# Optimization experiments

Hardware: AMD Instinct MI355X
Metric: run time of the kernel (lower is better)

The kernel has to match this reference:

```python
import jax, jax.numpy as jnp
import numpy as np

H = 2048        # hidden_size
E = 8           # num_experts
TOPK = 2
I = 1408        # moe_intermediate_size
IS = 5632       # shared_expert_intermediate_size
NORM_TOPK = True


def setup_inputs() -> dict:
    key = jax.random.key(0)
    ks = jax.random.split(key, 9)
    s = lambda k, shape: jax.random.normal(k, shape, dtype=jnp.float32) * (1.0 / np.sqrt(shape[-2] if len(shape) > 1 else shape[-1]))
    return {
        "hidden_states": jax.random.normal(ks[0], (1, 512, H), dtype=jnp.float32),
        "gate_w": jax.random.normal(ks[1], (E, H), dtype=jnp.float32) * 0.02,   # router Linear(H->E), no bias
        "w_gate": s(ks[2], (E, H, I)),   # expert gate_proj
        "w_up": s(ks[3], (E, H, I)),     # expert up_proj
        "w_down": s(ks[4], (E, I, H)),   # expert down_proj
        "sh_gate_w": s(ks[5], (H, IS)),  # shared expert gate_proj
        "sh_up_w": s(ks[6], (H, IS)),    # shared expert up_proj
        "sh_down_w": s(ks[7], (IS, H)),  # shared expert down_proj
        "shexp_gate_w": jax.random.normal(ks[8], (H, 1), dtype=jnp.float32) * 0.02,  # shared_expert_gate Linear(H->1)
    }


def reference(hidden_states, gate_w, w_gate, w_up, w_down,
              sh_gate_w, sh_up_w, sh_down_w, shexp_gate_w):
    B, S, _ = hidden_states.shape
    x = hidden_states.reshape(-1, H)                      # [T, H]
    T = x.shape[0]

    # --- router: softmax over all experts, then top-k (moe_gating_topk_softmax) ---
    router_logits = x @ gate_w.T                          # [T, E]
    probs = jax.nn.softmax(router_logits, axis=-1)
    routing_weights, selected_experts = jax.lax.top_k(probs, TOPK)  # [T, K]
    if NORM_TOPK:
        routing_weights = routing_weights / jnp.sum(routing_weights, axis=-1, keepdims=True)

    # dense combine weights: combine[t, e] = routing weight if expert e selected for token t else 0
    combine = jnp.zeros((T, E), dtype=x.dtype)
    combine = combine.at[jnp.arange(T)[:, None], selected_experts].set(routing_weights)

    # --- experts: SwiGLU MLP per expert, vectorized over E ---
    g = jnp.einsum('th,ehi->tei', x, w_gate)              # [T, E, I]
    u = jnp.einsum('th,ehi->tei', x, w_up)                # [T, E, I]
    h = jax.nn.silu(g) * u                                # [T, E, I]
    expert_out = jnp.einsum('tei,eih,te->th', h, w_down, combine)  # weighted scatter-add

    # --- shared expert with sigmoid gate ---
    sh = jax.nn.silu(x @ sh_gate_w) * (x @ sh_up_w)       # [T, IS]
    shared_out = (sh @ sh_down_w) * jax.nn.sigmoid(x @ shexp_gate_w)  # [T, H]

    out = (expert_out + shared_out).reshape(B, S, H)
    return (out, router_logits)
```

## Files before the change

### kernel.cpp

```cpp
#include <hip/hip_runtime.h>
#include <hip/hip_bf16.h>

#define NT  512
#define NH  2048
#define NE  8
#define NI  1408
#define NIS 5632

typedef __bf16 bf16x8 __attribute__((ext_vector_type(8)));
typedef float  f32x4  __attribute__((ext_vector_type(4)));

#define GLDS(gp, lp) __builtin_amdgcn_global_load_lds( \
    (const __attribute__((address_space(1))) void*)(gp), \
    (__attribute__((address_space(3))) void*)(lp), 16, 0, 0)

static constexpr size_t WS_XBF  = 0;
static constexpr size_t WS_SEL  = WS_XBF + (size_t)NT*NH*2;
static constexpr size_t WS_WTS  = WS_SEL + 4096;
static constexpr size_t WS_CNT  = WS_WTS + 4096;
static constexpr size_t WS_OFFE = WS_CNT + 32;
static constexpr size_t WS_TOK  = WS_OFFE + 32;
static constexpr size_t WS_PWT  = WS_TOK + 4096;
static constexpr size_t WS_SLOT = WS_PWT + 4096;
static constexpr size_t WS_G    = WS_SLOT + 4096;
static constexpr size_t WS_U    = WS_G   + (size_t)1024*NI*2;
static constexpr size_t WS_HBF  = WS_U   + (size_t)1024*NI*2;
static constexpr size_t WS_PAIR = WS_HBF + (size_t)1024*NI*2;
static constexpr size_t WS_SHG  = WS_PAIR+ (size_t)1024*NH*2;
static constexpr size_t WS_SHU  = WS_SHG + (size_t)NT*NIS*2;
static constexpr size_t WS_SHBF = WS_SHU + (size_t)NT*NIS*2;
static constexpr size_t WS_SHP  = WS_SHBF+ (size_t)NT*NIS*2;

__global__ void router_kernel(const float* __restrict__ x, const float* __restrict__ gw,
                              float* __restrict__ out_logits,
                              int* __restrict__ sel, float* __restrict__ wts)
{
    int w    = threadIdx.x >> 6;
    int lane = threadIdx.x & 63;
    int t    = blockIdx.x * 4 + w;
    int e    = lane & 7, c = lane >> 3;
    const float* xr = x  + (size_t)t * NH + c * 256;
    const float* gr = gw + (size_t)e * NH + c * 256;
    float acc = 0.f;
    #pragma unroll 8
    for (int it = 0; it < 64; ++it) {
        float4 xv = *(const float4*)(xr + it*4);
        float4 gv = *(const float4*)(gr + it*4);
        acc += xv.x*gv.x + xv.y*gv.y + xv.z*gv.z + xv.w*gv.w;
    }
    acc += __shfl_xor(acc, 8);
    acc += __shfl_xor(acc, 16);
    acc += __shfl_xor(acc, 32);
    if (lane < 8) out_logits[(size_t)t * NE + e] = acc;

    float l[8];
    #pragma unroll
    for (int j = 0; j < 8; ++j) l[j] = __shfl(acc, j);
    if (lane == 0) {
        int i1 = 0;
        #pragma unroll
        for (int j = 1; j < 8; ++j) if (l[j] > l[i1]) i1 = j;
        int i2 = -1;
        #pragma unroll
        for (int j = 0; j < 8; ++j) {
            if (j == i1) continue;
            if (i2 < 0 || l[j] > l[i2]) i2 = j;
        }
        float d  = expf(l[i2] - l[i1]);
        float w1 = 1.f / (1.f + d);
        float w2 = 1.f - w1;
        sel[2*t]   = i1;  sel[2*t+1] = i2;
        wts[2*t]   = w1;  wts[2*t+1] = w2;
    }
}

__global__ void bucket_kernel(const int* __restrict__ sel, const float* __restrict__ wts,
                              int* __restrict__ cnt, int* __restrict__ offe,
                              int* __restrict__ tok, float* __restrict__ pwt,
                              int* __restrict__ slot)
{
    int tid  = threadIdx.x;
    int wid  = tid >> 6;
    int lane = tid & 63;
    __shared__ int scnt[8], soff[8];

    unsigned long long masks[16];
    int total = 0;
    #pragma unroll
    for (int c = 0; c < 16; ++c) {
        int idx = c * 64 + lane;
        int s = sel[idx];
        unsigned long long m = __ballot(s == wid);
        masks[c] = m;
        total += __popcll(m);
    }
    if (lane == 0) { scnt[wid] = total; cnt[wid] = total; }
    __syncthreads();
    if (tid == 0) {
        int s = 0;
        #pragma unroll
        for (int j = 0; j < 8; ++j) { soff[j] = s; offe[j] = s; s += scnt[j]; }
    }
    __syncthreads();
    int pfx = soff[wid];
    unsigned long long below = (lane == 63) ? ~0ull >> 1 : ((1ull << lane) - 1);
    #pragma unroll
    for (int c = 0; c < 16; ++c) {
        int idx = c * 64 + lane;
        unsigned long long m = masks[c];
        if ((m >> lane) & 1ull) {
            int rank = pfx + (int)__popcll(m & below);
            tok[rank]  = idx >> 1;
            pwt[rank]  = wts[idx];
            slot[idx]  = rank;
        }
        pfx += (int)__popcll(m);
    }
}

__global__ void cast_kernel(const float* __restrict__ src, __bf16* __restrict__ dst, long long n)
{
    long long i = ((long long)blockIdx.x * blockDim.x + threadIdx.x) * 4;
    if (i >= n) return;
    float4 v = *(const float4*)(src + i);
    __bf16 o[4] = { (__bf16)v.x, (__bf16)v.y, (__bf16)v.z, (__bf16)v.w };
    *(uint2*)(dst + i) = *(const uint2*)o;
}

__global__ void silu_fused_kernel(const __bf16* __restrict__ g1, const __bf16* __restrict__ u1,
                                  __bf16* __restrict__ h1, long long n1,
                                  const __bf16* __restrict__ g2, const __bf16* __restrict__ u2,
                                  __bf16* __restrict__ h2, long long n2)
{
    long long i = ((long long)blockIdx.x * blockDim.x + threadIdx.x) * 8;
    const __bf16 *g, *u; __bf16* h; long long idx;
    if (i < n1)           { g = g1; u = u1; h = h1; idx = i; }
    else if (i < n1 + n2) { g = g2; u = u2; h = h2; idx = i - n1; }
    else return;
    uint4 gv = *(const uint4*)(g + idx);
    uint4 uv = *(const uint4*)(u + idx);
    const __bf16* gp = (const __bf16*)&gv;
    const __bf16* up = (const __bf16*)&uv;
    __bf16 o[8];
    #pragma unroll
    for (int j = 0; j < 8; ++j) {
        float x = (float)gp[j];
        float y = x / (1.f + __expf(-x)) * (float)up[j];
        o[j] = (__bf16)y;
    }
    *(uint4*)(h + idx) = *(const uint4*)o;
}

template<int NK, int LDB, bool GATHER>
__device__ __forceinline__ void gemm_core(char* __restrict__ smem,
    const __bf16* __restrict__ A, int lda,
    const float* __restrict__ B,
    __bf16* __restrict__ C, int ldc,
    int rows, int base, const int* __restrict__ tok, int m0, int n0)
{
    const int tid  = threadIdx.x;
    const int lane = tid & 63;
    const int wid  = tid >> 6;
    const int wr   = wid >> 1, wc = wid & 1;

    const int rs0 = (wid*2 + 0)*16 + (lane >> 2);
    const int rs1 = (wid*2 + 1)*16 + (lane >> 2);
    const int cch = lane & 3;
    int ga0 = m0 + rs0, ga1 = m0 + rs1;
    int ar0, ar1;
    if (GATHER) {
        ar0 = tok[base + (ga0 < rows ? ga0 : 0)];
        ar1 = tok[base + (ga1 < rows ? ga1 : 0)];
    } else {
        ar0 = base + (ga0 < rows ? ga0 : 0);
        ar1 = base + (ga1 < rows ? ga1 : 0);
    }
    const __bf16* a0p = A + (size_t)ar0 * lda + (cch ^ (rs0 & 3)) * 8;
    const __bf16* a1p = A + (size_t)ar1 * lda + (cch ^ (rs1 & 3)) * 8;

#define AGLDS(slot, t)                                               \
    {                                                                \
        char* d0 = smem + (slot)*8192 + (wid*2 + 0)*1024;            \
        char* d1 = smem + (slot)*8192 + (wid*2 + 1)*1024;            \
        GLDS(a0p + (size_t)(t)*32, d0);                              \
        GLDS(a1p + (size_t)(t)*32, d1);                              \
    }

    const int cn  = tid & 127;
    const int ckh = tid >> 7;
    const int csw = (cn >> 1) & 3;
    const float* bp = B + (size_t)(ckh * 16) * LDB + n0 + cn;
    char* bbuf0 = smem + 24576;
    char* bbuf1 = smem + 32768;

#define BLOAD(R, t)                                                  \
    {                                                                \
        const float* bq = bp + (size_t)(t) * 32 * LDB;               \
        _Pragma("unroll")                                            \
        for (int j = 0; j < 16; ++j) R[j] = bq[(size_t)j * LDB];     \
    }

#define CONVERT(R, bbase)                                            \
    {                                                                \
        __bf16 ob[16];                                               \
        _Pragma("unroll")                                            \
        for (int j = 0; j < 16; ++j) ob[j] = (__bf16)R[j];           \
        *(uint4*)((bbase) + cn*64 + (((ckh*2 + 0) ^ csw) * 16)) = ((const uint4*)ob)[0]; \
        *(uint4*)((bbase) + cn*64 + (((ckh*2 + 1) ^ csw) * 16)) = ((const uint4*)ob)[1]; \
    }

    const int fr = lane & 15, fq = lane >> 4;
    const int aoff = (wr*64 + fr)*64 + ((fq ^ (fr & 3)) * 16);
    const int boff = (wc*64 + fr)*64 + ((fq ^ ((fr >> 1) & 3)) * 16);

    f32x4 acc[4][4];
    #pragma unroll
    for (int i = 0; i < 4; ++i)
        #pragma unroll
        for (int j = 0; j < 4; ++j) acc[i][j] = f32x4{0.f,0.f,0.f,0.f};

#define MFMAS(slot, bbase)                                           \
    {                                                                \
        const char* Ab = smem + (slot)*8192;                         \
        bf16x8 af[4], bfr[4];                                        \
        _Pragma("unroll")                                            \
        for (int m = 0; m < 4; ++m) af[m]  = *(const bf16x8*)(Ab + aoff + m*1024); \
        _Pragma("unroll")                                            \
        for (int n = 0; n < 4; ++n) bfr[n] = *(const bf16x8*)((bbase) + boff + n*1024); \
        __builtin_amdgcn_s_setprio(1);                               \
        _Pragma("unroll")                                            \
        for (int m = 0; m < 4; ++m)                                  \
            _Pragma("unroll")                                        \
            for (int n = 0; n < 4; ++n)                              \
                acc[m][n] = __builtin_amdgcn_mfma_f32_16x16x32_bf16(af[m], bfr[n], acc[m][n], 0, 0, 0); \
        __builtin_amdgcn_s_setprio(0);                               \
    }

    float b0[16], b1[16];

    BLOAD(b0, 0); AGLDS(0, 0);
    BLOAD(b1, 1); AGLDS(1, 1);
    asm volatile("s_waitcnt vmcnt(18)" ::: "memory");
    CONVERT(b0, bbuf0);
    asm volatile("s_waitcnt lgkmcnt(0)" ::: "memory");
    __builtin_amdgcn_s_barrier();

    int sA = 0, sB = 1, sC = 2;
    #pragma unroll 1
    for (int t = 0; t < NK; t += 2) {
        if (t + 2 < NK) { BLOAD(b0, t + 2); AGLDS(sC, t + 2); }
        __builtin_amdgcn_sched_barrier(0);
        MFMAS(sA, bbuf0);
        __builtin_amdgcn_sched_barrier(0);
        if (t + 2 < NK) asm volatile("s_waitcnt vmcnt(18)" ::: "memory");
        else            asm volatile("s_waitcnt vmcnt(0)"  ::: "memory");
        CONVERT(b1, bbuf1);
        asm volatile("s_waitcnt lgkmcnt(0)" ::: "memory");
        __builtin_amdgcn_s_barrier();

        if (t + 3 < NK) { BLOAD(b1, t + 3); AGLDS(sA, t + 3); }
        __builtin_amdgcn_sched_barrier(0);
        MFMAS(sB, bbuf1);
        __builtin_amdgcn_sched_barrier(0);
        if (t + 2 < NK) {
            if (t + 3 < NK) asm volatile("s_waitcnt vmcnt(18)" ::: "memory");
            else            asm volatile("s_waitcnt vmcnt(0)"  ::: "memory");
            CONVERT(b0, bbuf0);
        }
        asm volatile("s_waitcnt lgkmcnt(0)" ::: "memory");
        __builtin_amdgcn_s_barrier();

        int tmp = sA; sA = sC; sC = sB; sB = tmp;
    }
#undef AGLDS
#undef BLOAD
#undef CONVERT
#undef MFMAS

    __bf16* ep = (__bf16*)(smem + wid * 9216);
    #pragma unroll
    for (int m = 0; m < 4; ++m)
        #pragma unroll
        for (int n = 0; n < 4; ++n)
            #pragma unroll
            for (int q = 0; q < 4; ++q)
                ep[(m*16 + fq*4 + q)*72 + n*16 + fr] = (__bf16)acc[m][n][q];

    const int grow = m0 + wr*64 + lane;
    if (grow < rows) {
        __bf16* cp = C + (size_t)(base + grow) * ldc + n0 + wc*64;
        const __bf16* rp = ep + lane * 72;
        #pragma unroll
        for (int j = 0; j < 8; ++j)
            *(uint4*)(cp + j*8) = *(const uint4*)(rp + j*8);
    }
}

__launch_bounds__(256, 3)
__global__ void gemm_p1(const __bf16* __restrict__ xbf,
                        const float* __restrict__ w_gate, const float* __restrict__ w_up,
                        const float* __restrict__ sh_gate, const float* __restrict__ sh_up,
                        __bf16* __restrict__ gbuf, __bf16* __restrict__ ubuf,
                        __bf16* __restrict__ shg, __bf16* __restrict__ shu,
                        const int* __restrict__ cnt, const int* __restrict__ offe,
                        const int* __restrict__ tok)
{
    __shared__ alignas(16) char smem[40960];
    int g = blockIdx.x;
    int x = g & 7;
    int j = g >> 3;
    if (j < 88) {
        int gu = j / 44;
        int r  = j % 44;
        int n  = r % 11;
        int m  = r / 11;
        int rows = cnt[x], base = offe[x];
        int m0 = m * 128; if (m0 >= rows) return;
        const float* B = (gu == 0 ? w_gate : w_up) + (size_t)x * NH * NI;
        __bf16* C = (gu == 0 ? gbuf : ubuf);
        gemm_core<NH/32, NI, true>(smem, xbf, NH, B, C, NI,
                                   rows, base, tok, m0, n * 128);
    } else {
        int s = j - 88;
        int z = s / 24;
        int rem = s % 24;
        int i = rem >> 2;
        int m = rem & 3;
        int n = x + 8 * i;
        if (n >= 44) return;
        const float* B = (z == 0 ? sh_gate : sh_up);
        __bf16* C = (z == 0 ? shg : shu);
        gemm_core<NH/32, NIS, false>(smem, xbf, NH, B, C, NIS,
                                     NT, 0, nullptr, m * 128, n * 128);
    }
}

__launch_bounds__(256, 3)
__global__ void gemm_p3(const __bf16* __restrict__ hbf, const __bf16* __restrict__ shbf,
                        const float* __restrict__ w_down, const float* __restrict__ sh_down,
                        __bf16* __restrict__ pair, __bf16* __restrict__ shp,
                        const int* __restrict__ cnt, const int* __restrict__ offe)
{
    __shared__ alignas(16) char smem[40960];
    int g = blockIdx.x;
    int x = g & 7;
    int j = g >> 3;
    if (j < 64) {
        int n = j % 16;
        int m = j / 16;
        int rows = cnt[x], base = offe[x];
        int m0 = m * 128; if (m0 >= rows) return;
        gemm_core<NI/32, NH, false>(smem, hbf, NI, w_down + (size_t)x * NI * NH,
                                    pair, NH, rows, base, nullptr, m0, n * 128);
    } else {
        int s = j - 64;
        int q = s >> 3;
        int rem = s & 7;
        int i = rem >> 2;
        int m = rem & 3;
        int n = x + 8 * i;
        gemm_core<NI/32, NH, false>(smem, shbf + q * NI, NIS,
                                    sh_down + (size_t)q * NI * NH,
                                    shp + (size_t)q * NT * NH, NH,
                                    NT, 0, nullptr, m * 128, n * 128);
    }
}

__global__ void combine_kernel(const float* __restrict__ x, const float* __restrict__ shexp_w,
                               const __bf16* __restrict__ shp, const __bf16* __restrict__ pair_out,
                               const int* __restrict__ slot, const float* __restrict__ wts,
                               float* __restrict__ out)
{
    int t = blockIdx.x;
    int tid = threadIdx.x;
    const float* xr = x + (size_t)t * NH;

    float p = 0.f;
    #pragma unroll
    for (int j = 0; j < 8; ++j) {
        int k = tid * 8 + j;
        p += xr[k] * shexp_w[k];
    }
    __shared__ float red[256];
    red[tid] = p;
    __syncthreads();
    for (int s = 128; s > 0; s >>= 1) {
        if (tid < s) red[tid] += red[tid + s];
        __syncthreads();
    }
    float sig = 1.f / (1.f + expf(-red[0]));

    int   s0 = slot[2*t],   s1 = slot[2*t+1];
    float w0 = wts[2*t],    w1 = wts[2*t+1];
    const __bf16* pr0 = pair_out + (size_t)s0 * NH;
    const __bf16* pr1 = pair_out + (size_t)s1 * NH;
    const __bf16* sd  = shp + (size_t)t * NH;
    float* orow = out + (size_t)t * NH;
    const size_t PS = (size_t)NT * NH;
    for (int n = tid; n < NH; n += 256) {
        float sdv = (float)sd[n] + (float)sd[n + PS] + (float)sd[n + 2*PS] + (float)sd[n + 3*PS];
        orow[n] = sdv * sig + w0 * (float)pr0[n] + w1 * (float)pr1[n];
    }
}

extern "C" void kernel_launch(void* const* d_in, const int* in_sizes, int n_in,
                              void* d_out, int out_size, void* d_ws, size_t ws_size,
                              hipStream_t stream)
{
    const float* x       = (const float*)d_in[0];
    const float* gate_w  = (const float*)d_in[1];
    const float* w_gate  = (const float*)d_in[2];
    const float* w_up    = (const float*)d_in[3];
    const float* w_down  = (const float*)d_in[4];
    const float* sh_gate = (const float*)d_in[5];
    const float* sh_up   = (const float*)d_in[6];
    const float* sh_down = (const float*)d_in[7];
    const float* shexp_g = (const float*)d_in[8];

    float* out        = (float*)d_out;
    float* out_logits = out + (size_t)NT * NH;

    char* ws = (char*)d_ws;
    __bf16* xbf  = (__bf16*)(ws + WS_XBF);
    int*    sel  = (int*)  (ws + WS_SEL);
    float*  wts  = (float*)(ws + WS_WTS);
    int*    cnt  = (int*)  (ws + WS_CNT);
    int*    offe = (int*)  (ws + WS_OFFE);
    int*    tok  = (int*)  (ws + WS_TOK);
    float*  pwt  = (float*)(ws + WS_PWT);
    int*    slot = (int*)  (ws + WS_SLOT);
    __bf16* gbuf = (__bf16*)(ws + WS_G);
    __bf16* ubuf = (__bf16*)(ws + WS_U);
    __bf16* hbf  = (__bf16*)(ws + WS_HBF);
    __bf16* pair = (__bf16*)(ws + WS_PAIR);
    __bf16* shg  = (__bf16*)(ws + WS_SHG);
    __bf16* shu  = (__bf16*)(ws + WS_SHU);
    __bf16* shbf = (__bf16*)(ws + WS_SHBF);
    __bf16* shp  = (__bf16*)(ws + WS_SHP);
    (void)pwt; (void)in_sizes; (void)n_in; (void)out_size; (void)ws_size;

    router_kernel<<<dim3(128), dim3(256), 0, stream>>>(x, gate_w, out_logits, sel, wts);
    bucket_kernel<<<dim3(1), dim3(512), 0, stream>>>(sel, wts, cnt, offe, tok, pwt, slot);
    cast_kernel<<<dim3(1024), dim3(256), 0, stream>>>(x, xbf, (long long)NT * NH);

    gemm_p1<<<dim3(1088), dim3(256), 0, stream>>>(
        xbf, w_gate, w_up, sh_gate, sh_up, gbuf, ubuf, shg, shu, cnt, offe, tok);

    silu_fused_kernel<<<dim3(2112), dim3(256), 0, stream>>>(
        gbuf, ubuf, hbf, (long long)1024 * NI,
        shg, shu, shbf, (long long)NT * NIS);

    gemm_p3<<<dim3(768), dim3(256), 0, stream>>>(
        hbf, shbf, w_down, sh_down, pair, shp, cnt, offe);

    combine_kernel<<<dim3(NT), dim3(256), 0, stream>>>(
        x, shexp_g, shp, pair, slot, wts, out);
}
```

Measured before the change: 199.6 us.

## Split-K the first GEMM phase in two and vectorize fp32 weight loads

The gate/up GEMMs (expert and shared) now split the K dimension into two halves, doubling the grid and writing bf16 partial sums to doubled workspace buffers. The SiLU kernel sums the two partials before applying the activation. Separately, the B-tile loader switches from 16 scalar strided loads per thread to 4 float4 loads with a new LDS store pattern, which lowers the outstanding-load counts in the waits. This aims for more parallelism and fewer memory instructions, at the cost of extra partial-result traffic and an extra bf16 rounding of the partial sums.

```diff
diff --git a/kernel.cpp b/kernel.cpp
--- a/kernel.cpp
+++ b/kernel.cpp
@@ -23,12 +23,12 @@
 static constexpr size_t WS_PWT  = WS_TOK + 4096;
 static constexpr size_t WS_SLOT = WS_PWT + 4096;
 static constexpr size_t WS_G    = WS_SLOT + 4096;
-static constexpr size_t WS_U    = WS_G   + (size_t)1024*NI*2;
-static constexpr size_t WS_HBF  = WS_U   + (size_t)1024*NI*2;
+static constexpr size_t WS_U    = WS_G   + (size_t)2*1024*NI*2;
+static constexpr size_t WS_HBF  = WS_U   + (size_t)2*1024*NI*2;
 static constexpr size_t WS_PAIR = WS_HBF + (size_t)1024*NI*2;
 static constexpr size_t WS_SHG  = WS_PAIR+ (size_t)1024*NH*2;
-static constexpr size_t WS_SHU  = WS_SHG + (size_t)NT*NIS*2;
-static constexpr size_t WS_SHBF = WS_SHU + (size_t)NT*NIS*2;
+static constexpr size_t WS_SHU  = WS_SHG + (size_t)2*NT*NIS*2;
+static constexpr size_t WS_SHBF = WS_SHU + (size_t)2*NT*NIS*2;
 static constexpr size_t WS_SHP  = WS_SHBF+ (size_t)NT*NIS*2;
 
 __global__ void router_kernel(const float* __restrict__ x, const float* __restrict__ gw,
@@ -128,24 +128,29 @@
 }
 
 __global__ void silu_fused_kernel(const __bf16* __restrict__ g1, const __bf16* __restrict__ u1,
-                                  __bf16* __restrict__ h1, long long n1,
+                                  __bf16* __restrict__ h1, long long n1, size_t ps1,
                                   const __bf16* __restrict__ g2, const __bf16* __restrict__ u2,
-                                  __bf16* __restrict__ h2, long long n2)
+                                  __bf16* __restrict__ h2, long long n2, size_t ps2)
 {
     long long i = ((long long)blockIdx.x * blockDim.x + threadIdx.x) * 8;
-    const __bf16 *g, *u; __bf16* h; long long idx;
-    if (i < n1)           { g = g1; u = u1; h = h1; idx = i; }
-    else if (i < n1 + n2) { g = g2; u = u2; h = h2; idx = i - n1; }
+    const __bf16 *g, *u; __bf16* h; long long idx; size_t ps;
+    if (i < n1)           { g = g1; u = u1; h = h1; idx = i;      ps = ps1; }
+    else if (i < n1 + n2) { g = g2; u = u2; h = h2; idx = i - n1; ps = ps2; }
     else return;
-    uint4 gv = *(const uint4*)(g + idx);
-    uint4 uv = *(const uint4*)(u + idx);
-    const __bf16* gp = (const __bf16*)&gv;
-    const __bf16* up = (const __bf16*)&uv;
+    uint4 gv0 = *(const uint4*)(g + idx);
+    uint4 gv1 = *(const uint4*)(g + idx + ps);
+    uint4 uv0 = *(const uint4*)(u + idx);
+    uint4 uv1 = *(const uint4*)(u + idx + ps);
+    const __bf16* gp0 = (const __bf16*)&gv0;
+    const __bf16* gp1 = (const __bf16*)&gv1;
+    const __bf16* up0 = (const __bf16*)&uv0;
+    const __bf16* up1 = (const __bf16*)&uv1;
     __bf16 o[8];
     #pragma unroll
     for (int j = 0; j < 8; ++j) {
-        float x = (float)gp[j];
-        float y = x / (1.f + __expf(-x)) * (float)up[j];
+        float xg = (float)gp0[j] + (float)gp1[j];
+        float xu = (float)up0[j] + (float)up1[j];
+        float y = xg / (1.f + __expf(-xg)) * xu;
         o[j] = (__bf16)y;
     }
     *(uint4*)(h + idx) = *(const uint4*)o;
@@ -186,10 +191,11 @@
         GLDS(a1p + (size_t)(t)*32, d1);                              \
     }
 
-    const int cn  = tid & 127;
-    const int ckh = tid >> 7;
-    const int csw = (cn >> 1) & 3;
-    const float* bp = B + (size_t)(ckh * 16) * LDB + n0 + cn;
+    const int cn4 = (tid & 31) * 4;
+    const int kr4 = (tid >> 5) * 4;
+    const int kck = kr4 >> 3;
+    const int kh  = (kr4 >> 2) & 1;
+    const float* bp = B + (size_t)kr4 * LDB + n0 + cn4;
     char* bbuf0 = smem + 24576;
     char* bbuf1 = smem + 32768;
 
@@ -197,16 +203,21 @@
     {                                                                \
         const float* bq = bp + (size_t)(t) * 32 * LDB;               \
         _Pragma("unroll")                                            \
-        for (int j = 0; j < 16; ++j) R[j] = bq[(size_t)j * LDB];     \
+        for (int j = 0; j < 4; ++j)                                  \
+            R[j] = *(const float4*)(bq + (size_t)j * LDB);           \
     }
 
 #define CONVERT(R, bbase)                                            \
     {                                                                \
-        __bf16 ob[16];                                               \
         _Pragma("unroll")                                            \
-        for (int j = 0; j < 16; ++j) ob[j] = (__bf16)R[j];           \
-        *(uint4*)((bbase) + cn*64 + (((ckh*2 + 0) ^ csw) * 16)) = ((const uint4*)ob)[0]; \
-        *(uint4*)((bbase) + cn*64 + (((ckh*2 + 1) ^ csw) * 16)) = ((const uint4*)ob)[1]; \
+        for (int c = 0; c < 4; ++c) {                                \
+            __bf16 ob[4];                                            \
+            _Pragma("unroll")                                        \
+            for (int j = 0; j < 4; ++j)                              \
+                ob[j] = (__bf16)(((const float*)(R))[j*4 + c]);      \
+            int col = cn4 + c;                                       \
+            *(uint2*)((bbase) + col*64 + ((kck ^ ((col>>1)&3)) * 16) + kh*8) = *(const uint2*)ob; \
+        }                                                            \
     }
 
     const int fr = lane & 15, fq = lane >> 4;
@@ -236,11 +247,11 @@
         __builtin_amdgcn_s_setprio(0);                               \
     }
 
-    float b0[16], b1[16];
+    float4 b0[4], b1[4];
 
     BLOAD(b0, 0); AGLDS(0, 0);
     BLOAD(b1, 1); AGLDS(1, 1);
-    asm volatile("s_waitcnt vmcnt(18)" ::: "memory");
+    asm volatile("s_waitcnt vmcnt(6)" ::: "memory");
     CONVERT(b0, bbuf0);
     asm volatile("s_waitcnt lgkmcnt(0)" ::: "memory");
     __builtin_amdgcn_s_barrier();
@@ -252,8 +263,8 @@
         __builtin_amdgcn_sched_barrier(0);
         MFMAS(sA, bbuf0);
         __builtin_amdgcn_sched_barrier(0);
-        if (t + 2 < NK) asm volatile("s_waitcnt vmcnt(18)" ::: "memory");
-        else            asm volatile("s_waitcnt vmcnt(0)"  ::: "memory");
+        if (t + 2 < NK) asm volatile("s_waitcnt vmcnt(6)" ::: "memory");
+        else            asm volatile("s_waitcnt vmcnt(0)" ::: "memory");
         CONVERT(b1, bbuf1);
         asm volatile("s_waitcnt lgkmcnt(0)" ::: "memory");
         __builtin_amdgcn_s_barrier();
@@ -263,8 +274,8 @@
         MFMAS(sB, bbuf1);
         __builtin_amdgcn_sched_barrier(0);
         if (t + 2 < NK) {
-            if (t + 3 < NK) asm volatile("s_waitcnt vmcnt(18)" ::: "memory");
-            else            asm volatile("s_waitcnt vmcnt(0)"  ::: "memory");
+            if (t + 3 < NK) asm volatile("s_waitcnt vmcnt(6)" ::: "memory");
+            else            asm volatile("s_waitcnt vmcnt(0)" ::: "memory");
             CONVERT(b0, bbuf0);
         }
         asm volatile("s_waitcnt lgkmcnt(0)" ::: "memory");
@@ -309,29 +320,33 @@
     int g = blockIdx.x;
     int x = g & 7;
     int j = g >> 3;
-    if (j < 88) {
-        int gu = j / 44;
-        int r  = j % 44;
-        int n  = r % 11;
-        int m  = r / 11;
+    if (j < 176) {
+        int gu = j / 88;
+        int r  = j % 88;
+        int k2 = r / 44;
+        int rr = r % 44;
+        int n  = rr % 11;
+        int m  = rr / 11;
         int rows = cnt[x], base = offe[x];
         int m0 = m * 128; if (m0 >= rows) return;
-        const float* B = (gu == 0 ? w_gate : w_up) + (size_t)x * NH * NI;
-        __bf16* C = (gu == 0 ? gbuf : ubuf);
-        gemm_core<NH/32, NI, true>(smem, xbf, NH, B, C, NI,
-                                   rows, base, tok, m0, n * 128);
+        const float* B = (gu == 0 ? w_gate : w_up) + (size_t)x * NH * NI + (size_t)k2 * 1024 * NI;
+        __bf16* C = (gu == 0 ? gbuf : ubuf) + (size_t)k2 * 1024 * NI;
+        gemm_core<32, NI, true>(smem, xbf + k2 * 1024, NH, B, C, NI,
+                                rows, base, tok, m0, n * 128);
     } else {
-        int s = j - 88;
-        int z = s / 24;
-        int rem = s % 24;
-        int i = rem >> 2;
-        int m = rem & 3;
+        int s = j - 176;
+        int z = s / 48;
+        int rem = s % 48;
+        int k2 = rem / 24;
+        int rem2 = rem % 24;
+        int i = rem2 >> 2;
+        int m = rem2 & 3;
         int n = x + 8 * i;
         if (n >= 44) return;
-        const float* B = (z == 0 ? sh_gate : sh_up);
-        __bf16* C = (z == 0 ? shg : shu);
-        gemm_core<NH/32, NIS, false>(smem, xbf, NH, B, C, NIS,
-                                     NT, 0, nullptr, m * 128, n * 128);
+        const float* B = (z == 0 ? sh_gate : sh_up) + (size_t)k2 * 1024 * NIS;
+        __bf16* C = (z == 0 ? shg : shu) + (size_t)k2 * NT * NIS;
+        gemm_core<32, NIS, false>(smem, xbf + k2 * 1024, NH, B, C, NIS,
+                                  NT, 0, nullptr, m * 128, n * 128);
     }
 }
 
@@ -443,12 +458,12 @@
     bucket_kernel<<<dim3(1), dim3(512), 0, stream>>>(sel, wts, cnt, offe, tok, pwt, slot);
     cast_kernel<<<dim3(1024), dim3(256), 0, stream>>>(x, xbf, (long long)NT * NH);
 
-    gemm_p1<<<dim3(1088), dim3(256), 0, stream>>>(
+    gemm_p1<<<dim3(2176), dim3(256), 0, stream>>>(
         xbf, w_gate, w_up, sh_gate, sh_up, gbuf, ubuf, shg, shu, cnt, offe, tok);
 
     silu_fused_kernel<<<dim3(2112), dim3(256), 0, stream>>>(
-        gbuf, ubuf, hbf, (long long)1024 * NI,
-        shg, shu, shbf, (long long)NT * NIS);
+        gbuf, ubuf, hbf, (long long)1024 * NI, (size_t)1024 * NI,
+        shg, shu, shbf, (long long)NT * NIS, (size_t)NT * NIS);
 
     gemm_p3<<<dim3(768), dim3(256), 0, stream>>>(
         hbf, shbf, w_down, sh_down, pair, shp, cnt, offe);
```

Result: slower. 214.7 us (+7.6%).

## Use 256-row tiles for shared-expert GEMMs and halve down-proj split-K

Applied to the files above, without the earlier changes.

Adds a gemm_core256 variant that computes 256x128 output tiles, so each fp32 weight tile loaded and converted to bf16 is reused across twice as many token rows. This is meant to halve the weight traffic and conversion work of the shared-expert GEMMs. The shared down projection now splits K into 2 parts instead of 4, so the combine kernel sums two partials. LDS grows to 64KB and launch bounds drop to 2 blocks per CU, which lowers occupancy and adds register pressure for all GEMM blocks in both kernels, including the routed-expert ones.

```diff
diff --git a/kernel.cpp b/kernel.cpp
--- a/kernel.cpp
+++ b/kernel.cpp
@@ -253,7 +253,7 @@
         MFMAS(sA, bbuf0);
         __builtin_amdgcn_sched_barrier(0);
         if (t + 2 < NK) asm volatile("s_waitcnt vmcnt(18)" ::: "memory");
-        else            asm volatile("s_waitcnt vmcnt(0)"  ::: "memory");
+        else            asm volatile("s_waitcnt vmcnt(0)" ::: "memory");
         CONVERT(b1, bbuf1);
         asm volatile("s_waitcnt lgkmcnt(0)" ::: "memory");
         __builtin_amdgcn_s_barrier();
@@ -264,7 +264,7 @@
         __builtin_amdgcn_sched_barrier(0);
         if (t + 2 < NK) {
             if (t + 3 < NK) asm volatile("s_waitcnt vmcnt(18)" ::: "memory");
-            else            asm volatile("s_waitcnt vmcnt(0)"  ::: "memory");
+            else            asm volatile("s_waitcnt vmcnt(0)" ::: "memory");
             CONVERT(b0, bbuf0);
         }
         asm volatile("s_waitcnt lgkmcnt(0)" ::: "memory");
@@ -296,7 +296,162 @@
     }
 }
 
-__launch_bounds__(256, 3)
+template<int NK, int LDB>
+__device__ __forceinline__ void gemm_core256(char* __restrict__ smem,
+    const __bf16* __restrict__ A, int lda,
+    const float* __restrict__ B,
+    __bf16* __restrict__ C, int ldc,
+    int rows, int m0, int n0)
+{
+    const int tid  = threadIdx.x;
+    const int lane = tid & 63;
+    const int wid  = tid >> 6;
+    const int wr   = wid >> 1, wc = wid & 1;
+
+    const int cch = lane & 3;
+    int rsv[4], arv[4];
+    #pragma unroll
+    for (int s = 0; s < 4; ++s) {
+        rsv[s] = (wid*4 + s)*16 + (lane >> 2);
+        int ga = m0 + rsv[s];
+        arv[s] = (ga < rows ? ga : 0);
+    }
+    const __bf16* ap0 = A + (size_t)arv[0] * lda + (cch ^ (rsv[0] & 3)) * 8;
+    const __bf16* ap1 = A + (size_t)arv[1] * lda + (cch ^ (rsv[1] & 3)) * 8;
+    const __bf16* ap2 = A + (size_t)arv[2] * lda + (cch ^ (rsv[2] & 3)) * 8;
+    const __bf16* ap3 = A + (size_t)arv[3] * lda + (cch ^ (rsv[3] & 3)) * 8;
+
+#define AGLDS2(slot, t)                                              \
+    {                                                                \
+        char* db = smem + (slot)*16384 + wid*4096;                   \
+        GLDS(ap0 + (size_t)(t)*32, db);                              \
+        GLDS(ap1 + (size_t)(t)*32, db + 1024);                       \
+        GLDS(ap2 + (size_t)(t)*32, db + 2048);                       \
+        GLDS(ap3 + (size_t)(t)*32, db + 3072);                       \
+    }
+
+    const int cn  = tid & 127;
+    const int ckh = tid >> 7;
+    const int csw = (cn >> 1) & 3;
+    const float* bp = B + (size_t)(ckh * 16) * LDB + n0 + cn;
+    char* bbuf0 = smem + 49152;
+    char* bbuf1 = smem + 57344;
+
+#define BLOAD2(R, t)                                                 \
+    {                                                                \
+        const float* bq = bp + (size_t)(t) * 32 * LDB;               \
+        _Pragma("unroll")                                            \
+        for (int j = 0; j < 16; ++j) R[j] = bq[(size_t)j * LDB];     \
+    }
+
+#define CONVERT2(R, bbase)                                           \
+    {                                                                \
+        __bf16 ob[16];                                               \
+        _Pragma("unroll")                                            \
+        for (int j = 0; j < 16; ++j) ob[j] = (__bf16)R[j];           \
+        *(uint4*)((bbase) + cn*64 + (((ckh*2 + 0) ^ csw) * 16)) = ((const uint4*)ob)[0]; \
+        *(uint4*)((bbase) + cn*64 + (((ckh*2 + 1) ^ csw) * 16)) = ((const uint4*)ob)[1]; \
+    }
+
+    const int fr = lane & 15, fq = lane >> 4;
+    const int asw = (fq ^ (fr & 3)) * 16;
+    const int boff = (wc*64 + fr)*64 + ((fq ^ ((fr >> 1) & 3)) * 16);
+
+    f32x4 acc[2][4][4];
+    #pragma unroll
+    for (int h = 0; h < 2; ++h)
+        #pragma unroll
+        for (int i = 0; i < 4; ++i)
+            #pragma unroll
+            for (int j = 0; j < 4; ++j) acc[h][i][j] = f32x4{0.f,0.f,0.f,0.f};
+
+#define MFMAS2(slot, bbase)                                          \
+    {                                                                \
+        const char* Ab = smem + (slot)*16384 + wr*8192;              \
+        bf16x8 af[8], bfr[4];                                        \
+        _Pragma("unroll")                                            \
+        for (int h = 0; h < 2; ++h)                                  \
+            _Pragma("unroll")                                        \
+            for (int m = 0; m < 4; ++m)                              \
+                af[h*4+m] = *(const bf16x8*)(Ab + (h*64 + m*16 + fr)*64 + asw); \
+        _Pragma("unroll")                                            \
+        for (int n = 0; n < 4; ++n) bfr[n] = *(const bf16x8*)((bbase) + boff + n*1024); \
+        __builtin_amdgcn_s_setprio(1);                               \
+        _Pragma("unroll")                                            \
+        for (int h = 0; h < 2; ++h)                                  \
+            _Pragma("unroll")                                        \
+            for (int m = 0; m < 4; ++m)                              \
+                _Pragma("unroll")                                    \
+                for (int n = 0; n < 4; ++n)                          \
+                    acc[h][m][n] = __builtin_amdgcn_mfma_f32_16x16x32_bf16(af[h*4+m], bfr[n], acc[h][m][n], 0, 0, 0); \
+        __builtin_amdgcn_s_setprio(0);                               \
+    }
+
+    float b0[16], b1[16];
+
+    BLOAD2(b0, 0); AGLDS2(0, 0);
+    BLOAD2(b1, 1); AGLDS2(1, 1);
+    asm volatile("s_waitcnt vmcnt(20)" ::: "memory");
+    CONVERT2(b0, bbuf0);
+    asm volatile("s_waitcnt lgkmcnt(0)" ::: "memory");
+    __builtin_amdgcn_s_barrier();
+
+    int sA = 0, sB = 1, sC = 2;
+    #pragma unroll 1
+    for (int t = 0; t < NK; t += 2) {
+        if (t + 2 < NK) { BLOAD2(b0, t + 2); AGLDS2(sC, t + 2); }
+        __builtin_amdgcn_sched_barrier(0);
+        MFMAS2(sA, bbuf0);
+        __builtin_amdgcn_sched_barrier(0);
+        if (t + 2 < NK) asm volatile("s_waitcnt vmcnt(20)" ::: "memory");
+        else            asm volatile("s_waitcnt vmcnt(0)" ::: "memory");
+        CONVERT2(b1, bbuf1);
+        asm volatile("s_waitcnt lgkmcnt(0)" ::: "memory");
+        __builtin_amdgcn_s_barrier();
+
+        if (t + 3 < NK) { BLOAD2(b1, t + 3); AGLDS2(sA, t + 3); }
+        __builtin_amdgcn_sched_barrier(0);
+        MFMAS2(sB, bbuf1);
+        __builtin_amdgcn_sched_barrier(0);
+        if (t + 2 < NK) {
+            if (t + 3 < NK) asm volatile("s_waitcnt vmcnt(20)" ::: "memory");
+            else            asm volatile("s_waitcnt vmcnt(0)" ::: "memory");
+            CONVERT2(b0, bbuf0);
+        }
+        asm volatile("s_waitcnt lgkmcnt(0)" ::: "memory");
+        __builtin_amdgcn_s_barrier();
+
+        int tmp = sA; sA = sC; sC = sB; sB = tmp;
+    }
+#undef AGLDS2
+#undef BLOAD2
+#undef CONVERT2
+#undef MFMAS2
+
+    __bf16* ep = (__bf16*)(smem + wid * 9216);
+    #pragma unroll 1
+    for (int h = 0; h < 2; ++h) {
+        asm volatile("s_waitcnt lgkmcnt(0)" ::: "memory");
+        #pragma unroll
+        for (int m = 0; m < 4; ++m)
+            #pragma unroll
+            for (int n = 0; n < 4; ++n)
+                #pragma unroll
+                for (int q = 0; q < 4; ++q)
+                    ep[(m*16 + fq*4 + q)*72 + n*16 + fr] =
+                        (__bf16)((h == 0 ? acc[0] : acc[1])[m][n][q]);
+        int grow = m0 + wr*128 + h*64 + lane;
+        if (grow < rows) {
+            __bf16* cp = C + (size_t)grow * ldc + n0 + wc*64;
+            const __bf16* rp = ep + lane * 72;
+            #pragma unroll
+            for (int j = 0; j < 8; ++j)
+                *(uint4*)(cp + j*8) = *(const uint4*)(rp + j*8);
+        }
+    }
+}
+
+__launch_bounds__(256, 2)
 __global__ void gemm_p1(const __bf16* __restrict__ xbf,
                         const float* __restrict__ w_gate, const float* __restrict__ w_up,
                         const float* __restrict__ sh_gate, const float* __restrict__ sh_up,
@@ -305,7 +460,7 @@
                         const int* __restrict__ cnt, const int* __restrict__ offe,
                         const int* __restrict__ tok)
 {
-    __shared__ alignas(16) char smem[40960];
+    __shared__ alignas(16) char smem[65536];
     int g = blockIdx.x;
     int x = g & 7;
     int j = g >> 3;
@@ -322,26 +477,26 @@
                                    rows, base, tok, m0, n * 128);
     } else {
         int s = j - 88;
-        int z = s / 24;
-        int rem = s % 24;
-        int i = rem >> 2;
-        int m = rem & 3;
+        int z = s / 12;
+        int rem = s % 12;
+        int i = rem >> 1;
+        int m = rem & 1;
         int n = x + 8 * i;
         if (n >= 44) return;
         const float* B = (z == 0 ? sh_gate : sh_up);
         __bf16* C = (z == 0 ? shg : shu);
-        gemm_core<NH/32, NIS, false>(smem, xbf, NH, B, C, NIS,
-                                     NT, 0, nullptr, m * 128, n * 128);
-    }
-}
-
-__launch_bounds__(256, 3)
+        gemm_core256<NH/32, NIS>(smem, xbf, NH, B, C, NIS,
+                                 NT, m * 256, n * 128);
+    }
+}
+
+__launch_bounds__(256, 2)
 __global__ void gemm_p3(const __bf16* __restrict__ hbf, const __bf16* __restrict__ shbf,
                         const float* __restrict__ w_down, const float* __restrict__ sh_down,
                         __bf16* __restrict__ pair, __bf16* __restrict__ shp,
                         const int* __restrict__ cnt, const int* __restrict__ offe)
 {
-    __shared__ alignas(16) char smem[40960];
+    __shared__ alignas(16) char smem[65536];
     int g = blockIdx.x;
     int x = g & 7;
     int j = g >> 3;
@@ -354,15 +509,15 @@
                                     pair, NH, rows, base, nullptr, m0, n * 128);
     } else {
         int s = j - 64;
-        int q = s >> 3;
-        int rem = s & 7;
-        int i = rem >> 2;
-        int m = rem & 3;
+        int q = s >> 2;
+        int rem = s & 3;
+        int i = rem >> 1;
+        int m = rem & 1;
         int n = x + 8 * i;
-        gemm_core<NI/32, NH, false>(smem, shbf + q * NI, NIS,
-                                    sh_down + (size_t)q * NI * NH,
-                                    shp + (size_t)q * NT * NH, NH,
-                                    NT, 0, nullptr, m * 128, n * 128);
+        gemm_core256<NIS/64, NH>(smem, shbf + (size_t)q * (NIS/2), NIS,
+                                 sh_down + (size_t)q * (NIS/2) * NH,
+                                 shp + (size_t)q * NT * NH, NH,
+                                 NT, m * 256, n * 128);
     }
 }
 
@@ -398,7 +553,7 @@
     float* orow = out + (size_t)t * NH;
     const size_t PS = (size_t)NT * NH;
     for (int n = tid; n < NH; n += 256) {
-        float sdv = (float)sd[n] + (float)sd[n + PS] + (float)sd[n + 2*PS] + (float)sd[n + 3*PS];
+        float sdv = (float)sd[n] + (float)sd[n + PS];
         orow[n] = sdv * sig + w0 * (float)pr0[n] + w1 * (float)pr1[n];
     }
 }
@@ -443,14 +598,14 @@
     bucket_kernel<<<dim3(1), dim3(512), 0, stream>>>(sel, wts, cnt, offe, tok, pwt, slot);
     cast_kernel<<<dim3(1024), dim3(256), 0, stream>>>(x, xbf, (long long)NT * NH);
 
-    gemm_p1<<<dim3(1088), dim3(256), 0, stream>>>(
+    gemm_p1<<<dim3(896), dim3(256), 0, stream>>>(
         xbf, w_gate, w_up, sh_gate, sh_up, gbuf, ubuf, shg, shu, cnt, offe, tok);
 
     silu_fused_kernel<<<dim3(2112), dim3(256), 0, stream>>>(
         gbuf, ubuf, hbf, (long long)1024 * NI,
         shg, shu, shbf, (long long)NT * NIS);
 
-    gemm_p3<<<dim3(768), dim3(256), 0, stream>>>(
+    gemm_p3<<<dim3(576), dim3(256), 0, stream>>>(
         hbf, shbf, w_down, sh_down, pair, shp, cnt, offe);
 
     combine_kernel<<<dim3(NT), dim3(256), 0, stream>>>(
```

New measurement: 285.5 us. 1.43x slower.
